# Performance work log

Hardware: AMD Instinct MI355X
Metric: run time of the kernel (lower is better)

Reference implementation:

```python
import jax, jax.numpy as jnp
import numpy as np
from jax import lax

D_MODEL = 1024
D_STATE = 16
D_CONV = 4
EXPAND = 2
D_INNER = D_MODEL * EXPAND
B, T = 2, 1024


def setup_inputs() -> dict:
    key = jax.random.key(0)
    ks = jax.random.split(key, 8)
    s = 0.02
    x = jax.random.normal(ks[0], (B, T, D_MODEL), dtype=jnp.float32)
    in_proj_w = jax.random.normal(ks[1], (D_MODEL, 2 * D_INNER), dtype=jnp.float32) * s
    conv_w = jax.random.normal(ks[2], (D_INNER, 1, D_CONV), dtype=jnp.float32) * s  # depthwise [O, I/G=1, K]
    conv_b = jax.random.normal(ks[3], (D_INNER,), dtype=jnp.float32) * s
    x_proj_w = jax.random.normal(ks[4], (D_INNER, 2 * D_STATE + 1), dtype=jnp.float32) * s
    dt_proj_w = jax.random.normal(ks[5], (1, D_INNER), dtype=jnp.float32) * s
    dt_proj_b = jax.random.normal(ks[6], (D_INNER,), dtype=jnp.float32) * s
    # Canonical Mamba init: A_log = log(1..d_state) broadcast over d_inner
    A_log = jnp.broadcast_to(jnp.log(jnp.arange(1, D_STATE + 1, dtype=jnp.float32))[None, :], (D_INNER, D_STATE))
    D_param = jnp.ones((D_INNER,), dtype=jnp.float32)
    c_proj_w = jax.random.normal(ks[7], (D_INNER, D_MODEL), dtype=jnp.float32) * s
    return {"x": x, "in_proj_w": in_proj_w, "conv_w": conv_w, "conv_b": conv_b,
            "x_proj_w": x_proj_w, "dt_proj_w": dt_proj_w, "dt_proj_b": dt_proj_b,
            "A_log": A_log, "D_param": D_param, "c_proj_w": c_proj_w}


def _mamba_fwd(x, in_proj_w, conv_w, conv_b, x_proj_w, dt_proj_w, dt_proj_b, A_log, D_param, c_proj_w):
    Bb, Tt, _ = x.shape
    xz = jnp.einsum('btd,de->bte', x, in_proj_w)          # [B,T,2*Di]
    x_branch, z = jnp.split(xz, 2, axis=-1)               # [B,T,Di] each
    # Causal depthwise conv1d: pad left K-1 (== torch pad both + slice[:T])
    xb = jnp.transpose(x_branch, (0, 2, 1))               # [B,Di,T]
    xb = lax.conv_general_dilated(xb, conv_w, window_strides=(1,),
                                  padding=[(D_CONV - 1, 0)],
                                  feature_group_count=D_INNER,
                                  dimension_numbers=('NCH', 'OIH', 'NCH'))
    xb = xb + conv_b[None, :, None]
    x_branch = jax.nn.silu(jnp.transpose(xb, (0, 2, 1)))  # [B,T,Di]
    x_ssm = jnp.einsum('btd,dk->btk', x_branch, x_proj_w) # [B,T,2S+1]
    B_t = x_ssm[:, :, :D_STATE]                            # [B,T,S]
    C_t = x_ssm[:, :, D_STATE:2 * D_STATE]                 # [B,T,S]
    dt = x_ssm[:, :, -1:]                                  # [B,T,1]
    dt = jax.nn.softplus(jnp.einsum('btk,kd->btd', dt, dt_proj_w) + dt_proj_b)  # [B,T,Di]
    A = -jnp.exp(A_log)                                    # [Di,S]
    A_bar = jnp.exp(dt[..., None] * A[None, None])         # [B,T,Di,S]
    Bx = (dt[..., None] * B_t[:, :, None, :]) * x_branch[..., None]  # [B,T,Di,S]

    def step(h, inp):
        a, bx, c = inp                                     # [B,Di,S],[B,Di,S],[B,S]
        h = a * h + bx
        y = jnp.einsum('bds,bs->bd', h, c)
        return h, y

    h0 = jnp.zeros((Bb, D_INNER, D_STATE), dtype=x.dtype)
    _, ys = lax.scan(step, h0,
                     (jnp.transpose(A_bar, (1, 0, 2, 3)),
                      jnp.transpose(Bx, (1, 0, 2, 3)),
                      jnp.transpose(C_t, (1, 0, 2))))
    y = jnp.transpose(ys, (1, 0, 2))                       # [B,T,Di]
    y = y + D_param[None, None, :] * x_branch
    y = y * jax.nn.silu(z)
    return jnp.einsum('btd,de->bte', y, c_proj_w)          # [B,T,d_model]


def reference(x, in_proj_w, conv_w, conv_b, x_proj_w, dt_proj_w, dt_proj_b, A_log, D_param, c_proj_w):
    return _mamba_fwd(x, in_proj_w, conv_w, conv_b, x_proj_w, dt_proj_w, dt_proj_b, A_log, D_param, c_proj_w)
```

## Files before the change

kernel.cpp:

```cpp
#include <hip/hip_runtime.h>
#include <math.h>

#define DMODEL 1024
#define DSTATE 16
#define DCONV 4
#define DINNER 2048
#define BATCH 2
#define SEQ 1024
#define BT (BATCH*SEQ)
#define NC 32
#define LC 32

typedef unsigned short ushort_t;
typedef __attribute__((ext_vector_type(8))) short short8;
typedef __attribute__((ext_vector_type(4))) float f32x4;

__device__ __forceinline__ ushort_t f2bf(float f) {
    union { float f; unsigned int u; } v; v.f = f;
    unsigned int r = v.u + 0x7fffu + ((v.u >> 16) & 1u);
    return (ushort_t)(r >> 16);
}

__device__ __forceinline__ float softplusf(float x) {
    return (x > 20.f) ? x : log1pf(__expf(x));
}

#define GLOAD_LDS16(G, L) \
  __builtin_amdgcn_global_load_lds((const __attribute__((address_space(1))) void*)(G), \
                                   (__attribute__((address_space(3))) void*)(L), 16, 0, 0)

__global__ __launch_bounds__(256) void cast_bf16_kernel(const float* __restrict__ in,
                                                        ushort_t* __restrict__ out,
                                                        float* __restrict__ zp)
{
    size_t i = ((size_t)blockIdx.x * 256 + threadIdx.x) * 8;
    float4 a = *(const float4*)&in[i];
    float4 b = *(const float4*)&in[i + 4];
    uint4 p;
    p.x = (unsigned)f2bf(a.x) | ((unsigned)f2bf(a.y) << 16);
    p.y = (unsigned)f2bf(a.z) | ((unsigned)f2bf(a.w) << 16);
    p.z = (unsigned)f2bf(b.x) | ((unsigned)f2bf(b.y) << 16);
    p.w = (unsigned)f2bf(b.z) | ((unsigned)f2bf(b.w) << 16);
    *(uint4*)&out[i] = p;
    if (blockIdx.x < 66) {
        size_t z = ((size_t)blockIdx.x * 256 + threadIdx.x) * 4;
        *(float4*)&zp[z] = make_float4(0.f, 0.f, 0.f, 0.f);
    }
}

__global__ __launch_bounds__(256) void transpose_cast_kernel(const float* __restrict__ in,
                                                             ushort_t* __restrict__ out,
                                                             int R, int Cc)
{
    __shared__ float t[32][33];
    const int r0 = blockIdx.y * 32;
    const int c0 = blockIdx.x * 32;
    const int tid = threadIdx.x;
    {
        int lr = tid >> 3, lc4 = (tid & 7) * 4;
        float4 v = *(const float4*)&in[(size_t)(r0 + lr) * Cc + c0 + lc4];
        t[lr][lc4 + 0] = v.x; t[lr][lc4 + 1] = v.y;
        t[lr][lc4 + 2] = v.z; t[lr][lc4 + 3] = v.w;
    }
    __syncthreads();
    {
        int oc = tid >> 3, rq = (tid & 7) * 4;
        ushort4 u;
        u.x = f2bf(t[rq + 0][oc]);
        u.y = f2bf(t[rq + 1][oc]);
        u.z = f2bf(t[rq + 2][oc]);
        u.w = f2bf(t[rq + 3][oc]);
        *(ushort4*)&out[(size_t)(c0 + oc) * R + r0 + rq] = u;
    }
}

template<int BM, int BN>
__global__ __launch_bounds__(256) void gemm_bt(const ushort_t* __restrict__ A,
                                               const ushort_t* __restrict__ Bt,
                                               float* __restrict__ C,
                                               int M, int N, int K)
{
    constexpr int BK = 64;
    constexpr int AL = BM * BK / (256 * 8);
    constexpr int BL = BN * BK / (256 * 8);
    constexpr int FM = BM / 32;
    constexpr int FN = BN / 32;
    __shared__ __align__(16) ushort_t Al[BM * BK];
    __shared__ __align__(16) ushort_t Bl[BN * BK];

    const int tid  = threadIdx.x;
    const int lane = tid & 63;
    const int wid  = tid >> 6;
    const int wr   = wid >> 1;
    const int wc   = wid & 1;
    const int bm   = blockIdx.y * BM;
    const int bn   = blockIdx.x * BN;

    f32x4 acc[FM][FN] = {};

    for (int k0 = 0; k0 < K; k0 += BK) {
#pragma unroll
        for (int j = 0; j < AL; j++) {
            int chunk = j * 256 + tid;
            GLOAD_LDS16(&A[(size_t)(bm + (chunk >> 3)) * K + k0 + (chunk & 7) * 8],
                        &Al[(size_t)(j * 256 + wid * 64) * 8]);
        }
#pragma unroll
        for (int j = 0; j < BL; j++) {
            int chunk = j * 256 + tid;
            GLOAD_LDS16(&Bt[(size_t)(bn + (chunk >> 3)) * K + k0 + (chunk & 7) * 8],
                        &Bl[(size_t)(j * 256 + wid * 64) * 8]);
        }
        __syncthreads();

#pragma unroll
        for (int kk = 0; kk < 2; kk++) {
            short8 af[FM], bf[FN];
#pragma unroll
            for (int m = 0; m < FM; m++)
                af[m] = *(const short8*)&Al[(wr * (BM / 2) + m * 16 + (lane & 15)) * BK
                                            + (lane >> 4) * 8 + kk * 32];
#pragma unroll
            for (int n = 0; n < FN; n++)
                bf[n] = *(const short8*)&Bl[(wc * (BN / 2) + n * 16 + (lane & 15)) * BK
                                            + (lane >> 4) * 8 + kk * 32];
#pragma unroll
            for (int m = 0; m < FM; m++)
#pragma unroll
                for (int n = 0; n < FN; n++)
                    acc[m][n] = __builtin_amdgcn_mfma_f32_16x16x32_bf16(af[m], bf[n], acc[m][n], 0, 0, 0);
        }
        __syncthreads();
    }

#pragma unroll
    for (int m = 0; m < FM; m++)
#pragma unroll
        for (int n = 0; n < FN; n++) {
            int row0 = bm + wr * (BM / 2) + m * 16 + (lane >> 4) * 4;
            int col  = bn + wc * (BN / 2) + n * 16 + (lane & 15);
#pragma unroll
            for (int r = 0; r < 4; r++)
                C[(size_t)(row0 + r) * N + col] = acc[m][n][r];
        }
}

__global__ __launch_bounds__(256) void conv_silu_kernel(const float* __restrict__ xz,
                                                        const float* __restrict__ cw,
                                                        const float* __restrict__ cb,
                                                        float* __restrict__ xb_rm)
{
    __shared__ float tile[64 + 3][64];
    const int b  = blockIdx.z;
    const int t0 = blockIdx.x * 64;
    const int d0 = blockIdx.y * 64;
    const int tid = threadIdx.x;

    for (int e = tid; e < 67 * 16; e += 256) {
        int r  = e / 16;
        int c4 = (e % 16) * 4;
        int t  = t0 - 3 + r;
        float4 v = make_float4(0.f, 0.f, 0.f, 0.f);
        if (t >= 0)
            v = *(const float4*)&xz[((size_t)b * SEQ + t) * (2 * DINNER) + d0 + c4];
        *(float4*)&tile[r][c4] = v;
    }
    __syncthreads();

    const int dl = tid & 63;
    const int tb = tid >> 6;
    const int d  = d0 + dl;
    const float w0 = cw[d * 4 + 0], w1 = cw[d * 4 + 1];
    const float w2 = cw[d * 4 + 2], w3 = cw[d * 4 + 3];
    const float bias = cb[d];

#pragma unroll
    for (int ii = 0; ii < 16; ii++) {
        int tl = tb + 4 * ii;
        float s = bias;
        s = fmaf(tile[tl + 0][dl], w0, s);
        s = fmaf(tile[tl + 1][dl], w1, s);
        s = fmaf(tile[tl + 2][dl], w2, s);
        s = fmaf(tile[tl + 3][dl], w3, s);
        float sil = s / (1.f + __expf(-s));
        xb_rm[((size_t)b * SEQ + t0 + tl) * DINNER + d] = sil;
    }
}

__global__ __launch_bounds__(256) void xproj_kernel(const float* __restrict__ xb,
                                                    const float* __restrict__ w,
                                                    float* __restrict__ Btb,
                                                    float* __restrict__ Ctb,
                                                    float* __restrict__ dtraw)
{
    __shared__ float xs[8][256];
    __shared__ float ws[256][33];
    const int bt0 = blockIdx.x * 8;
    const int kc  = blockIdx.y * 256;
    const int tid = threadIdx.x;
    const int r = tid >> 5, n = tid & 31;

#pragma unroll
    for (int j = 0; j < 2; j++) {
        int e4 = (j * 256 + tid) * 4;
        int rr = e4 >> 8, cc = e4 & 255;
        *(float4*)&xs[rr][cc] = *(const float4*)&xb[(size_t)(bt0 + rr) * DINNER + kc + cc];
    }
    {
        const float* wsrc = w + (size_t)kc * 33;
        float* wdst = &ws[0][0];
        for (int e4 = tid; e4 < 2112; e4 += 256)
            *(float4*)&wdst[e4 * 4] = *(const float4*)&wsrc[e4 * 4];
    }
    __syncthreads();

    float acc = 0.f;
#pragma unroll 16
    for (int kk = 0; kk < 256; kk += 4) {
        float4 xv = *(const float4*)&xs[r][kk];
        acc = fmaf(xv.x, ws[kk + 0][n], acc);
        acc = fmaf(xv.y, ws[kk + 1][n], acc);
        acc = fmaf(xv.z, ws[kk + 2][n], acc);
        acc = fmaf(xv.w, ws[kk + 3][n], acc);
    }
    float dacc = 0.f;
#pragma unroll
    for (int j = 0; j < 8; j++)
        dacc = fmaf(xs[r][n * 8 + j], ws[n * 8 + j][32], dacc);
#pragma unroll
    for (int off = 16; off; off >>= 1)
        dacc += __shfl_xor(dacc, off, 32);

    if (n < 16) atomicAdd(&Btb[(bt0 + r) * 16 + n], acc);
    else        atomicAdd(&Ctb[(bt0 + r) * 16 + (n - 16)], acc);
    if (n == 0) atomicAdd(&dtraw[bt0 + r], dacc);
}

__device__ __forceinline__ void qpowers(float q, float* a)
{
    float q2 = q * q, q4 = q2 * q2, q8 = q4 * q4;
    a[0] = q;        a[1] = q2;       a[2] = q2 * q;   a[3] = q4;
    a[4] = q4 * q;   a[5] = q4 * q2;  a[6] = q4 * a[2];a[7] = q8;
    a[8] = q8 * q;   a[9] = q8 * q2;  a[10]= q8 * a[2];a[11]= q8 * q4;
    a[12]= q8 * a[4];a[13]= q8 * a[5];a[14]= q8 * a[6];a[15]= q8 * q8;
}

__device__ __forceinline__ bool a_structure_ok(const float* A_log, int d, float As2_0)
{
    bool ok = true;
#pragma unroll
    for (int s = 1; s < 16; s++) {
        float v = -__expf(A_log[d * 16 + s]) * 1.44269504f;
        ok &= (fabsf(v - (float)(s + 1) * As2_0) <= 1e-4f * (float)(s + 1) * fabsf(As2_0));
    }
    return ok;
}

__global__ __launch_bounds__(256) void scan1_kernel(const float* __restrict__ xb,
                                                    const float* __restrict__ dtraw,
                                                    const float* __restrict__ Btb,
                                                    const float* __restrict__ A_log,
                                                    const float* __restrict__ dtw,
                                                    const float* __restrict__ dtb,
                                                    float* __restrict__ Hend,
                                                    float* __restrict__ dtsum)
{
    __shared__ float raw[LC];
    __shared__ float xs[LC][256];
    __shared__ float Bs[LC][16];

    const int tid = threadIdx.x;
    const int c   = blockIdx.x;
    const int b   = blockIdx.z;
    const int d0  = blockIdx.y * 256;
    const int d   = d0 + tid;
    const int t0  = c * LC;

    if (tid < LC / 4)
        *(float4*)&raw[tid * 4] = *(const float4*)&dtraw[b * SEQ + t0 + tid * 4];
    if (tid < 128)
        *(float4*)&Bs[0][tid * 4] = *(const float4*)&Btb[((size_t)b * SEQ + t0) * 16 + tid * 4];
#pragma unroll
    for (int j = 0; j < 8; j++) {
        int e = j * 256 + tid;
        int rr = e >> 6, c4 = (e & 63) * 4;
        *(float4*)&xs[rr][c4] = *(const float4*)&xb[((size_t)b * SEQ + t0 + rr) * DINNER + d0 + c4];
    }

    const float wd = dtw[d], bd = dtb[d];
    const float As2_0 = -__expf(A_log[d * 16]) * 1.44269504f;
    const bool fast = a_structure_ok(A_log, d, As2_0);

    float h[16];
#pragma unroll
    for (int s = 0; s < 16; s++) h[s] = 0.f;
    float dsum = 0.f;
    __syncthreads();

    if (fast) {
#pragma unroll 2
        for (int t = 0; t < LC; t++) {
            float dt = softplusf(fmaf(raw[t], wd, bd));
            float xv = xs[t][tid];
            float Bv[16];
#pragma unroll
            for (int s4 = 0; s4 < 4; s4++)
                *(float4*)&Bv[s4 * 4] = *(const float4*)&Bs[t][s4 * 4];
            float a[16];
            qpowers(exp2f(dt * As2_0), a);
            float dtx = dt * xv;
            dsum += dt;
#pragma unroll
            for (int s = 0; s < 16; s++)
                h[s] = fmaf(a[s], h[s], Bv[s] * dtx);
        }
    } else {
        float As2[16];
#pragma unroll
        for (int s = 0; s < 16; s++)
            As2[s] = -__expf(A_log[d * 16 + s]) * 1.44269504f;
#pragma unroll 2
        for (int t = 0; t < LC; t++) {
            float dt = softplusf(fmaf(raw[t], wd, bd));
            float xv = xs[t][tid];
            float Bv[16];
#pragma unroll
            for (int s4 = 0; s4 < 4; s4++)
                *(float4*)&Bv[s4 * 4] = *(const float4*)&Bs[t][s4 * 4];
            float dtx = dt * xv;
            dsum += dt;
#pragma unroll
            for (int s = 0; s < 16; s++)
                h[s] = fmaf(exp2f(dt * As2[s]), h[s], Bv[s] * dtx);
        }
    }

    size_t hb = (((size_t)b * NC + c) * DINNER + d) * 16;
#pragma unroll
    for (int s4 = 0; s4 < 4; s4++)
        *(float4*)&Hend[hb + s4 * 4] = *(float4*)&h[s4 * 4];
    dtsum[((size_t)b * NC + c) * DINNER + d] = dsum;
}

__global__ __launch_bounds__(256) void carry_kernel(const float* __restrict__ Hend,
                                                    const float* __restrict__ dtsum,
                                                    const float* __restrict__ A_log,
                                                    float* __restrict__ Hstart)
{
    const int idx = blockIdx.x * 256 + threadIdx.x;
    const int s = idx & 15;
    const int d = (idx >> 4) & (DINNER - 1);
    const int b = idx >> 15;
    const float As2 = -__expf(A_log[d * 16 + s]) * 1.44269504f;
    float hs = 0.f;
    for (int c = 0; c < NC; c++) {
        size_t off = ((size_t)b * NC + c);
        float P  = exp2f(As2 * dtsum[off * DINNER + d]);
        size_t hi = (off * DINNER + d) * 16 + s;
        float he = Hend[hi];
        Hstart[hi] = hs;
        hs = fmaf(P, hs, he);
    }
}

__global__ __launch_bounds__(256) void scan3_kernel(const float* __restrict__ xb,
                                                    const float* __restrict__ dtraw,
                                                    const float* __restrict__ Btb,
                                                    const float* __restrict__ Ctb,
                                                    const float* __restrict__ A_log,
                                                    const float* __restrict__ dtw,
                                                    const float* __restrict__ dtb,
                                                    const float* __restrict__ Hstart,
                                                    const float* __restrict__ xz,
                                                    const float* __restrict__ Dp,
                                                    ushort_t* __restrict__ ygb)
{
    __shared__ float raw[LC];
    __shared__ float xs[LC][256];
    __shared__ float Bs[LC][16];
    __shared__ float Cs[LC][16];

    const int tid = threadIdx.x;
    const int c   = blockIdx.x;
    const int b   = blockIdx.z;
    const int d0  = blockIdx.y * 256;
    const int d   = d0 + tid;
    const int t0  = c * LC;

    if (tid < LC / 4)
        *(float4*)&raw[tid * 4] = *(const float4*)&dtraw[b * SEQ + t0 + tid * 4];
    if (tid < 128)
        *(float4*)&Bs[0][tid * 4] = *(const float4*)&Btb[((size_t)b * SEQ + t0) * 16 + tid * 4];
    else {
        int u = tid - 128;
        *(float4*)&Cs[0][u * 4] = *(const float4*)&Ctb[((size_t)b * SEQ + t0) * 16 + u * 4];
    }
#pragma unroll
    for (int j = 0; j < 8; j++) {
        int e = j * 256 + tid;
        int rr = e >> 6, c4 = (e & 63) * 4;
        *(float4*)&xs[rr][c4] = *(const float4*)&xb[((size_t)b * SEQ + t0 + rr) * DINNER + d0 + c4];
    }

    const float wd = dtw[d], bd = dtb[d];
    const float Dd = Dp[d];
    const float As2_0 = -__expf(A_log[d * 16]) * 1.44269504f;
    const bool fast = a_structure_ok(A_log, d, As2_0);

    float h[16];
    {
        size_t hb = (((size_t)b * NC + c) * DINNER + d) * 16;
#pragma unroll
        for (int s4 = 0; s4 < 4; s4++)
            *(float4*)&h[s4 * 4] = *(const float4*)&Hstart[hb + s4 * 4];
    }
    __syncthreads();

    if (fast) {
#pragma unroll 2
        for (int t = 0; t < LC; t++) {
            float dt = softplusf(fmaf(raw[t], wd, bd));
            float xv = xs[t][tid];
            float Bv[16], Cv[16];
#pragma unroll
            for (int s4 = 0; s4 < 4; s4++) {
                *(float4*)&Bv[s4 * 4] = *(const float4*)&Bs[t][s4 * 4];
                *(float4*)&Cv[s4 * 4] = *(const float4*)&Cs[t][s4 * 4];
            }
            float a[16];
            qpowers(exp2f(dt * As2_0), a);
            float dtx = dt * xv;
            float acc = 0.f;
#pragma unroll
            for (int s = 0; s < 16; s++) {
                h[s] = fmaf(a[s], h[s], Bv[s] * dtx);
                acc = fmaf(h[s], Cv[s], acc);
            }
            xs[t][tid] = fmaf(Dd, xv, acc);
        }
    } else {
        float As2[16];
#pragma unroll
        for (int s = 0; s < 16; s++)
            As2[s] = -__expf(A_log[d * 16 + s]) * 1.44269504f;
#pragma unroll 2
        for (int t = 0; t < LC; t++) {
            float dt = softplusf(fmaf(raw[t], wd, bd));
            float xv = xs[t][tid];
            float Bv[16], Cv[16];
#pragma unroll
            for (int s4 = 0; s4 < 4; s4++) {
                *(float4*)&Bv[s4 * 4] = *(const float4*)&Bs[t][s4 * 4];
                *(float4*)&Cv[s4 * 4] = *(const float4*)&Cs[t][s4 * 4];
            }
            float dtx = dt * xv;
            float acc = 0.f;
#pragma unroll
            for (int s = 0; s < 16; s++) {
                h[s] = fmaf(exp2f(dt * As2[s]), h[s], Bv[s] * dtx);
                acc = fmaf(h[s], Cv[s], acc);
            }
            xs[t][tid] = fmaf(Dd, xv, acc);
        }
    }
    __syncthreads();

#pragma unroll
    for (int j = 0; j < 8; j++) {
        int e = j * 256 + tid;
        int rr = e >> 6, c4 = (e & 63) * 4;
        float4 yv = *(const float4*)&xs[rr][c4];
        float4 zv = *(const float4*)&xz[((size_t)b * SEQ + t0 + rr) * (2 * DINNER) + DINNER + d0 + c4];
        ushort4 u;
        u.x = f2bf(yv.x * (zv.x / (1.f + __expf(-zv.x))));
        u.y = f2bf(yv.y * (zv.y / (1.f + __expf(-zv.y))));
        u.z = f2bf(yv.z * (zv.z / (1.f + __expf(-zv.z))));
        u.w = f2bf(yv.w * (zv.w / (1.f + __expf(-zv.w))));
        *(ushort4*)&ygb[((size_t)b * SEQ + t0 + rr) * DINNER + d0 + c4] = u;
    }
}

extern "C" void kernel_launch(void* const* d_in, const int* in_sizes, int n_in,
                              void* d_out, int out_size, void* d_ws, size_t ws_size,
                              hipStream_t stream)
{
    const float* x         = (const float*)d_in[0];
    const float* in_proj_w = (const float*)d_in[1];
    const float* conv_w    = (const float*)d_in[2];
    const float* conv_b    = (const float*)d_in[3];
    const float* x_proj_w  = (const float*)d_in[4];
    const float* dt_proj_w = (const float*)d_in[5];
    const float* dt_proj_b = (const float*)d_in[6];
    const float* A_log     = (const float*)d_in[7];
    const float* D_param   = (const float*)d_in[8];
    const float* c_proj_w  = (const float*)d_in[9];
    float* out = (float*)d_out;

    float* ws    = (float*)d_ws;
    float* xz    = ws;
    float* xb    = xz  + (size_t)BT * 4096;
    float* Btb   = xb  + (size_t)BT * DINNER;
    float* Ctb   = Btb + (size_t)BT * 16;
    float* dtraw = Ctb + (size_t)BT * 16;
    float* Hend  = dtraw + BT;
    float* Hstart= Hend + (size_t)BATCH * NC * DINNER * 16;
    float* dtsum = Hstart + (size_t)BATCH * NC * DINNER * 16;
    ushort_t* xbf = (ushort_t*)(dtsum + (size_t)BATCH * NC * DINNER);
    ushort_t* w1T = xbf + (size_t)BT * DMODEL;
    ushort_t* w2T = w1T + (size_t)(2 * DINNER) * DMODEL;
    ushort_t* ygb = w2T + (size_t)DMODEL * DINNER;

    cast_bf16_kernel<<<dim3((BT * DMODEL) / (8 * 256)), 256, 0, stream>>>(x, xbf, Btb);
    transpose_cast_kernel<<<dim3((2 * DINNER) / 32, DMODEL / 32), 256, 0, stream>>>(
        in_proj_w, w1T, DMODEL, 2 * DINNER);
    transpose_cast_kernel<<<dim3(DMODEL / 32, DINNER / 32), 256, 0, stream>>>(
        c_proj_w, w2T, DINNER, DMODEL);

    gemm_bt<128, 128><<<dim3((2 * DINNER) / 128, BT / 128), 256, 0, stream>>>(
        xbf, w1T, xz, BT, 2 * DINNER, DMODEL);

    conv_silu_kernel<<<dim3(SEQ / 64, DINNER / 64, BATCH), 256, 0, stream>>>(
        xz, conv_w, conv_b, xb);

    xproj_kernel<<<dim3(BT / 8, 8), 256, 0, stream>>>(xb, x_proj_w, Btb, Ctb, dtraw);

    scan1_kernel<<<dim3(NC, DINNER / 256, BATCH), 256, 0, stream>>>(
        xb, dtraw, Btb, A_log, dt_proj_w, dt_proj_b, Hend, dtsum);
    carry_kernel<<<dim3(BATCH * DINNER * 16 / 256), 256, 0, stream>>>(
        Hend, dtsum, A_log, Hstart);
    scan3_kernel<<<dim3(NC, DINNER / 256, BATCH), 256, 0, stream>>>(
        xb, dtraw, Btb, Ctb, A_log, dt_proj_w, dt_proj_b, Hstart, xz, D_param, ygb);

    gemm_bt<64, 128><<<dim3(DMODEL / 128, BT / 64), 256, 0, stream>>>(
        ygb, w2T, out, BT, DMODEL, DINNER);
}
```

Measured before the change: 173.3 us.

## Fuse prep kernels, silu(z) into in-proj epilogue, and carry pass into scan1

Merges the input cast and both weight transpose-casts into one prep launch. A dedicated in-projection GEMM writes the x half compactly and stores silu(z) as bf16, so scan3 reads half the bytes and no longer computes the exponential. The separate carry kernel is replaced by a last-block-done pattern in scan1 that uses atomic counters, removing a launch but running the serial chunk carry inside one block per group. The output GEMM tile also shrinks to 64x64 to launch more blocks. Storing silu(z) in bf16 adds rounding error.

Result: slower. 254.2 us (+46.7%).

```diff
diff --git a/kernel.cpp b/kernel.cpp
--- a/kernel.cpp
+++ b/kernel.cpp
@@ -20,7 +20,10 @@
     unsigned int r = v.u + 0x7fffu + ((v.u >> 16) & 1u);
     return (ushort_t)(r >> 16);
 }
-
+__device__ __forceinline__ float bf2f(ushort_t u) {
+    union { unsigned int u; float f; } v; v.u = ((unsigned int)u) << 16;
+    return v.f;
+}
 __device__ __forceinline__ float softplusf(float x) {
     return (x > 20.f) ? x : log1pf(__expf(x));
 }
@@ -29,33 +32,47 @@
   __builtin_amdgcn_global_load_lds((const __attribute__((address_space(1))) void*)(G), \
                                    (__attribute__((address_space(3))) void*)(L), 16, 0, 0)
 
-__global__ __launch_bounds__(256) void cast_bf16_kernel(const float* __restrict__ in,
-                                                        ushort_t* __restrict__ out,
-                                                        float* __restrict__ zp)
-{
-    size_t i = ((size_t)blockIdx.x * 256 + threadIdx.x) * 8;
-    float4 a = *(const float4*)&in[i];
-    float4 b = *(const float4*)&in[i + 4];
-    uint4 p;
-    p.x = (unsigned)f2bf(a.x) | ((unsigned)f2bf(a.y) << 16);
-    p.y = (unsigned)f2bf(a.z) | ((unsigned)f2bf(a.w) << 16);
-    p.z = (unsigned)f2bf(b.x) | ((unsigned)f2bf(b.y) << 16);
-    p.w = (unsigned)f2bf(b.z) | ((unsigned)f2bf(b.w) << 16);
-    *(uint4*)&out[i] = p;
-    if (blockIdx.x < 66) {
-        size_t z = ((size_t)blockIdx.x * 256 + threadIdx.x) * 4;
-        *(float4*)&zp[z] = make_float4(0.f, 0.f, 0.f, 0.f);
-    }
-}
-
-__global__ __launch_bounds__(256) void transpose_cast_kernel(const float* __restrict__ in,
-                                                             ushort_t* __restrict__ out,
-                                                             int R, int Cc)
+__global__ __launch_bounds__(256) void prep_kernel(const float* __restrict__ x,
+                                                   ushort_t* __restrict__ xbf,
+                                                   const float* __restrict__ w1,
+                                                   ushort_t* __restrict__ w1T,
+                                                   const float* __restrict__ w2,
+                                                   ushort_t* __restrict__ w2T,
+                                                   float* __restrict__ zacc,
+                                                   int* __restrict__ counters)
 {
     __shared__ float t[32][33];
-    const int r0 = blockIdx.y * 32;
-    const int c0 = blockIdx.x * 32;
+    const int bid = blockIdx.x;
     const int tid = threadIdx.x;
+
+    if (bid < 1024) {
+        size_t i = ((size_t)bid * 256 + tid) * 8;
+        float4 a = *(const float4*)&x[i];
+        float4 b = *(const float4*)&x[i + 4];
+        uint4 p;
+        p.x = (unsigned)f2bf(a.x) | ((unsigned)f2bf(a.y) << 16);
+        p.y = (unsigned)f2bf(a.z) | ((unsigned)f2bf(a.w) << 16);
+        p.z = (unsigned)f2bf(b.x) | ((unsigned)f2bf(b.y) << 16);
+        p.w = (unsigned)f2bf(b.z) | ((unsigned)f2bf(b.w) << 16);
+        *(uint4*)&xbf[i] = p;
+        if (bid < 66) {
+            size_t z = ((size_t)bid * 256 + tid) * 4;
+            *(float4*)&zacc[z] = make_float4(0.f, 0.f, 0.f, 0.f);
+        }
+        if (bid == 1023 && tid < 16) counters[tid] = 0;
+        return;
+    }
+
+    const float* in; ushort_t* out; int R, Cc, r0, c0;
+    if (bid < 5120) {
+        int b2 = bid - 1024;
+        in = w1; out = w1T; R = DMODEL; Cc = 2 * DINNER;
+        r0 = (b2 >> 7) * 32; c0 = (b2 & 127) * 32;
+    } else {
+        int b3 = bid - 5120;
+        in = w2; out = w2T; R = DINNER; Cc = DMODEL;
+        r0 = (b3 >> 5) * 32; c0 = (b3 & 31) * 32;
+    }
     {
         int lr = tid >> 3, lc4 = (tid & 7) * 4;
         float4 v = *(const float4*)&in[(size_t)(r0 + lr) * Cc + c0 + lc4];
@@ -74,6 +91,92 @@
     }
 }
 
+__global__ __launch_bounds__(256) void gemm_in(const ushort_t* __restrict__ A,
+                                               const ushort_t* __restrict__ Bt,
+                                               float* __restrict__ xzx,
+                                               ushort_t* __restrict__ zsil)
+{
+    constexpr int BM = 128, BN = 128, BK = 64;
+    constexpr int AL = BM * BK / (256 * 8);
+    constexpr int BL = BN * BK / (256 * 8);
+    constexpr int FM = BM / 32;
+    constexpr int FN = BN / 32;
+    const int K = DMODEL, N = 2 * DINNER;
+    __shared__ __align__(16) ushort_t Al[BM * BK];
+    __shared__ __align__(16) ushort_t Bl[BN * BK];
+
+    const int tid  = threadIdx.x;
+    const int lane = tid & 63;
+    const int wid  = tid >> 6;
+    const int wr   = wid >> 1;
+    const int wc   = wid & 1;
+    const int bm   = blockIdx.y * BM;
+    const int bn   = blockIdx.x * BN;
+
+    f32x4 acc[FM][FN] = {};
+
+    for (int k0 = 0; k0 < K; k0 += BK) {
+#pragma unroll
+        for (int j = 0; j < AL; j++) {
+            int chunk = j * 256 + tid;
+            GLOAD_LDS16(&A[(size_t)(bm + (chunk >> 3)) * K + k0 + (chunk & 7) * 8],
+                        &Al[(size_t)(j * 256 + wid * 64) * 8]);
+        }
+#pragma unroll
+        for (int j = 0; j < BL; j++) {
+            int chunk = j * 256 + tid;
+            GLOAD_LDS16(&Bt[(size_t)(bn + (chunk >> 3)) * K + k0 + (chunk & 7) * 8],
+                        &Bl[(size_t)(j * 256 + wid * 64) * 8]);
+        }
+        __syncthreads();
+
+#pragma unroll
+        for (int kk = 0; kk < 2; kk++) {
+            short8 af[FM], bf[FN];
+#pragma unroll
+            for (int m = 0; m < FM; m++)
+                af[m] = *(const short8*)&Al[(wr * (BM / 2) + m * 16 + (lane & 15)) * BK
+                                            + (lane >> 4) * 8 + kk * 32];
+#pragma unroll
+            for (int n = 0; n < FN; n++)
+                bf[n] = *(const short8*)&Bl[(wc * (BN / 2) + n * 16 + (lane & 15)) * BK
+                                            + (lane >> 4) * 8 + kk * 32];
+#pragma unroll
+            for (int m = 0; m < FM; m++)
+#pragma unroll
+                for (int n = 0; n < FN; n++)
+                    acc[m][n] = __builtin_amdgcn_mfma_f32_16x16x32_bf16(af[m], bf[n], acc[m][n], 0, 0, 0);
+        }
+        __syncthreads();
+    }
+
+    if (bn < DINNER) {
+#pragma unroll
+        for (int m = 0; m < FM; m++)
+#pragma unroll
+            for (int n = 0; n < FN; n++) {
+                int row0 = bm + wr * (BM / 2) + m * 16 + (lane >> 4) * 4;
+                int col  = bn + wc * (BN / 2) + n * 16 + (lane & 15);
+#pragma unroll
+                for (int r = 0; r < 4; r++)
+                    xzx[(size_t)(row0 + r) * DINNER + col] = acc[m][n][r];
+            }
+    } else {
+#pragma unroll
+        for (int m = 0; m < FM; m++)
+#pragma unroll
+            for (int n = 0; n < FN; n++) {
+                int row0 = bm + wr * (BM / 2) + m * 16 + (lane >> 4) * 4;
+                int col  = bn - DINNER + wc * (BN / 2) + n * 16 + (lane & 15);
+#pragma unroll
+                for (int r = 0; r < 4; r++) {
+                    float z = acc[m][n][r];
+                    zsil[(size_t)(row0 + r) * DINNER + col] = f2bf(z / (1.f + __expf(-z)));
+                }
+            }
+    }
+}
+
 template<int BM, int BN>
 __global__ __launch_bounds__(256) void gemm_bt(const ushort_t* __restrict__ A,
                                                const ushort_t* __restrict__ Bt,
@@ -145,7 +248,7 @@
         }
 }
 
-__global__ __launch_bounds__(256) void conv_silu_kernel(const float* __restrict__ xz,
+__global__ __launch_bounds__(256) void conv_silu_kernel(const float* __restrict__ xzx,
                                                         const float* __restrict__ cw,
                                                         const float* __restrict__ cb,
                                                         float* __restrict__ xb_rm)
@@ -162,7 +265,7 @@
         int t  = t0 - 3 + r;
         float4 v = make_float4(0.f, 0.f, 0.f, 0.f);
         if (t >= 0)
-            v = *(const float4*)&xz[((size_t)b * SEQ + t) * (2 * DINNER) + d0 + c4];
+            v = *(const float4*)&xzx[((size_t)b * SEQ + t) * DINNER + d0 + c4];
         *(float4*)&tile[r][c4] = v;
     }
     __syncthreads();
@@ -263,11 +366,14 @@
                                                     const float* __restrict__ dtw,
                                                     const float* __restrict__ dtb,
                                                     float* __restrict__ Hend,
-                                                    float* __restrict__ dtsum)
+                                                    float* __restrict__ dtsum,
+                                                    float* __restrict__ Hstart,
+                                                    int* __restrict__ counters)
 {
     __shared__ float raw[LC];
     __shared__ float xs[LC][256];
     __shared__ float Bs[LC][16];
+    __shared__ int lastflag;
 
     const int tid = threadIdx.x;
     const int c   = blockIdx.x;
@@ -340,26 +446,36 @@
     for (int s4 = 0; s4 < 4; s4++)
         *(float4*)&Hend[hb + s4 * 4] = *(float4*)&h[s4 * 4];
     dtsum[((size_t)b * NC + c) * DINNER + d] = dsum;
-}
-
-__global__ __launch_bounds__(256) void carry_kernel(const float* __restrict__ Hend,
-                                                    const float* __restrict__ dtsum,
-                                                    const float* __restrict__ A_log,
-                                                    float* __restrict__ Hstart)
-{
-    const int idx = blockIdx.x * 256 + threadIdx.x;
-    const int s = idx & 15;
-    const int d = (idx >> 4) & (DINNER - 1);
-    const int b = idx >> 15;
-    const float As2 = -__expf(A_log[d * 16 + s]) * 1.44269504f;
-    float hs = 0.f;
-    for (int c = 0; c < NC; c++) {
-        size_t off = ((size_t)b * NC + c);
-        float P  = exp2f(As2 * dtsum[off * DINNER + d]);
-        size_t hi = (off * DINNER + d) * 16 + s;
-        float he = Hend[hi];
-        Hstart[hi] = hs;
-        hs = fmaf(P, hs, he);
+
+    __threadfence();
+    if (tid == 0) {
+        int grp = b * (DINNER / 256) + blockIdx.y;
+        lastflag = (atomicAdd(&counters[grp], 1) == NC - 1);
+    }
+    __syncthreads();
+    if (lastflag) {
+        __threadfence();
+        float hs[16], As2r[16];
+        int dArr[16], sArr[16];
+#pragma unroll
+        for (int j = 0; j < 16; j++) {
+            int p = tid + 256 * j;
+            dArr[j] = d0 + (p >> 4);
+            sArr[j] = p & 15;
+            As2r[j] = -__expf(A_log[dArr[j] * 16 + sArr[j]]) * 1.44269504f;
+            hs[j] = 0.f;
+        }
+        for (int c2 = 0; c2 < NC; c2++) {
+            size_t off = (size_t)b * NC + c2;
+#pragma unroll
+            for (int j = 0; j < 16; j++) {
+                float P = exp2f(As2r[j] * dtsum[off * DINNER + dArr[j]]);
+                size_t hi = (off * DINNER + dArr[j]) * 16 + sArr[j];
+                float he = Hend[hi];
+                Hstart[hi] = hs[j];
+                hs[j] = fmaf(P, hs[j], he);
+            }
+        }
     }
 }
 
@@ -371,7 +487,7 @@
                                                     const float* __restrict__ dtw,
                                                     const float* __restrict__ dtb,
                                                     const float* __restrict__ Hstart,
-                                                    const float* __restrict__ xz,
+                                                    const ushort_t* __restrict__ zsil,
                                                     const float* __restrict__ Dp,
                                                     ushort_t* __restrict__ ygb)
 {
@@ -470,12 +586,12 @@
         int e = j * 256 + tid;
         int rr = e >> 6, c4 = (e & 63) * 4;
         float4 yv = *(const float4*)&xs[rr][c4];
-        float4 zv = *(const float4*)&xz[((size_t)b * SEQ + t0 + rr) * (2 * DINNER) + DINNER + d0 + c4];
+        ushort4 zv = *(const ushort4*)&zsil[((size_t)b * SEQ + t0 + rr) * DINNER + d0 + c4];
         ushort4 u;
-        u.x = f2bf(yv.x * (zv.x / (1.f + __expf(-zv.x))));
-        u.y = f2bf(yv.y * (zv.y / (1.f + __expf(-zv.y))));
-        u.z = f2bf(yv.z * (zv.z / (1.f + __expf(-zv.z))));
-        u.w = f2bf(yv.w * (zv.w / (1.f + __expf(-zv.w))));
+        u.x = f2bf(yv.x * bf2f(zv.x));
+        u.y = f2bf(yv.y * bf2f(zv.y));
+        u.z = f2bf(yv.z * bf2f(zv.z));
+        u.w = f2bf(yv.w * bf2f(zv.w));
         *(ushort4*)&ygb[((size_t)b * SEQ + t0 + rr) * DINNER + d0 + c4] = u;
     }
 }
@@ -497,40 +613,38 @@
     float* out = (float*)d_out;
 
     float* ws    = (float*)d_ws;
-    float* xz    = ws;
-    float* xb    = xz  + (size_t)BT * 4096;
+    float* xzx   = ws;
+    float* xb    = xzx + (size_t)BT * DINNER;
     float* Btb   = xb  + (size_t)BT * DINNER;
     float* Ctb   = Btb + (size_t)BT * 16;
     float* dtraw = Ctb + (size_t)BT * 16;
     float* Hend  = dtraw + BT;
     float* Hstart= Hend + (size_t)BATCH * NC * DINNER * 16;
     float* dtsum = Hstart + (size_t)BATCH * NC * DINNER * 16;
-    ushort_t* xbf = (ushort_t*)(dtsum + (size_t)BATCH * NC * DINNER);
-    ushort_t* w1T = xbf + (size_t)BT * DMODEL;
-    ushort_t* w2T = w1T + (size_t)(2 * DINNER) * DMODEL;
-    ushort_t* ygb = w2T + (size_t)DMODEL * DINNER;
-
-    cast_bf16_kernel<<<dim3((BT * DMODEL) / (8 * 256)), 256, 0, stream>>>(x, xbf, Btb);
-    transpose_cast_kernel<<<dim3((2 * DINNER) / 32, DMODEL / 32), 256, 0, stream>>>(
-        in_proj_w, w1T, DMODEL, 2 * DINNER);
-    transpose_cast_kernel<<<dim3(DMODEL / 32, DINNER / 32), 256, 0, stream>>>(
-        c_proj_w, w2T, DINNER, DMODEL);
-
-    gemm_bt<128, 128><<<dim3((2 * DINNER) / 128, BT / 128), 256, 0, stream>>>(
-        xbf, w1T, xz, BT, 2 * DINNER, DMODEL);
+    int*   counters = (int*)(dtsum + (size_t)BATCH * NC * DINNER);
+    ushort_t* xbf  = (ushort_t*)(counters + 16);
+    ushort_t* w1T  = xbf + (size_t)BT * DMODEL;
+    ushort_t* w2T  = w1T + (size_t)(2 * DINNER) * DMODEL;
+    ushort_t* ygb  = w2T + (size_t)DMODEL * DINNER;
+    ushort_t* zsil = ygb + (size_t)BT * DINNER;
+
+    prep_kernel<<<dim3(1024 + 4096 + 2048), 256, 0, stream>>>(
+        x, xbf, in_proj_w, w1T, c_proj_w, w2T, Btb, counters);
+
+    gemm_in<<<dim3((2 * DINNER) / 128, BT / 128), 256, 0, stream>>>(
+        xbf, w1T, xzx, zsil);
 
     conv_silu_kernel<<<dim3(SEQ / 64, DINNER / 64, BATCH), 256, 0, stream>>>(
-        xz, conv_w, conv_b, xb);
+        xzx, conv_w, conv_b, xb);
 
     xproj_kernel<<<dim3(BT / 8, 8), 256, 0, stream>>>(xb, x_proj_w, Btb, Ctb, dtraw);
 
     scan1_kernel<<<dim3(NC, DINNER / 256, BATCH), 256, 0, stream>>>(
-        xb, dtraw, Btb, A_log, dt_proj_w, dt_proj_b, Hend, dtsum);
-    carry_kernel<<<dim3(BATCH * DINNER * 16 / 256), 256, 0, stream>>>(
-        Hend, dtsum, A_log, Hstart);
+        xb, dtraw, Btb, A_log, dt_proj_w, dt_proj_b, Hend, dtsum, Hstart, counters);
+
     scan3_kernel<<<dim3(NC, DINNER / 256, BATCH), 256, 0, stream>>>(
-        xb, dtraw, Btb, Ctb, A_log, dt_proj_w, dt_proj_b, Hstart, xz, D_param, ygb);
-
-    gemm_bt<64, 128><<<dim3(DMODEL / 128, BT / 64), 256, 0, stream>>>(
+        xb, dtraw, Btb, Ctb, A_log, dt_proj_w, dt_proj_b, Hstart, zsil, D_param, ygb);
+
+    gemm_bt<64, 64><<<dim3(DMODEL / 64, BT / 64), 256, 0, stream>>>(
         ygb, w2T, out, BT, DMODEL, DINNER);
 }
```
